# Performance work log

Measured on AMD Instinct MI355X. Metric: run time of the kernel, lower is better.

The kernel has to match this reference:

```python
import jax, jax.numpy as jnp
import numpy as np

K = 3  # kernel side; ori_col = K*K = 9


def _build_tpcms():
    # order-2: all pairs (i, j), i <= j, over the 9 patch positions
    pairs2 = []
    idx2 = {}
    c = 0
    for i in range(K * K):
        for j in range(i, K * K):
            pairs2.append((i, j))
            idx2[(i, j)] = c
            c += 1
    # order-3: (raw column index i, index of (j, k) in the order-2 tensor), i <= j <= k
    pairs3 = [(i, idx2[(j, k)])
              for i in range(K * K)
              for j in range(i, K * K)
              for k in range(j, K * K)]
    return np.asarray(pairs2, np.int32), np.asarray(pairs3, np.int32)


def setup_inputs() -> dict:
    key = jax.random.key(0)
    x = jax.random.normal(key, (4, 8, 128, 128), dtype=jnp.float32)
    p2, p3 = _build_tpcms()
    return {"x": x, "tpcm2": jnp.asarray(p2), "tpcm3": jnp.asarray(p3)}


def _unfold3x3(x):
    # torch.nn.Unfold(kernel=3, stride=1, pad=1) then view(B, C, 9, L):
    # per channel, the 9 kernel offsets are row-major (kh, kw).
    B, C, H, W = x.shape
    xp = jnp.pad(x, ((0, 0), (0, 0), (1, 1), (1, 1)))
    cols = [xp[:, :, i:i + H, j:j + W] for i in range(K) for j in range(K)]
    return jnp.stack(cols, axis=2).reshape(B, C, K * K, H * W)  # [B, C, 9, L]


def reference(x, tpcm2, tpcm3):
    Col = _unfold3x3(x)                                          # [B, C, 9, L]
    ht2 = Col[:, :, tpcm2[:, 0], :] * Col[:, :, tpcm2[:, 1], :]  # [B, C, 45, L]
    ht3 = Col[:, :, tpcm3[:, 0], :] * ht2[:, :, tpcm3[:, 1], :]  # [B, C, 165, L]
    return jnp.concatenate([ht2, ht3], axis=2)                   # [B, C, 210, L]
```

## Files before the change

### kernel.cpp

```cpp
#include <hip/hip_runtime.h>


#define HH 128
#define WW 128
#define LL (HH * WW)
#define NCH 210

__global__ __launch_bounds__(256) void hoi_kernel(const float* __restrict__ x,
                                                  float* __restrict__ out) {
    const int tid   = blockIdx.x * 256 + threadIdx.x;
    const int wq    = tid & 31;
    const int h     = (tid >> 5) & 127;
    const int plane = tid >> 12;
    const int w0    = wq << 2;

    const float* __restrict__ xp = x + (size_t)plane * LL;

    float r[3][6];
#pragma unroll
    for (int dh = 0; dh < 3; ++dh) {
        const int hh = h + dh - 1;
        const bool hv = (hh >= 0) & (hh < HH);
#pragma unroll
        for (int dw = 0; dw < 6; ++dw) {
            const int ww = w0 + dw - 1;
            const bool wv = (ww >= 0) & (ww < WW);
            r[dh][dw] = (hv & wv) ? xp[hh * WW + ww] : 0.0f;
        }
    }

    float4 v[9];
#pragma unroll
    for (int dh = 0; dh < 3; ++dh) {
#pragma unroll
        for (int dw = 0; dw < 3; ++dw) {
            v[dh * 3 + dw] = make_float4(r[dh][dw], r[dh][dw + 1],
                                         r[dh][dw + 2], r[dh][dw + 3]);
        }
    }

    float* __restrict__ obase = out + (size_t)plane * NCH * LL + h * WW + w0;
    int ch = 0;

#pragma unroll
    for (int i = 0; i < 9; ++i) {
#pragma unroll
        for (int j = i; j < 9; ++j) {
            float4 p;
            p.x = v[i].x * v[j].x;
            p.y = v[i].y * v[j].y;
            p.z = v[i].z * v[j].z;
            p.w = v[i].w * v[j].w;
            *reinterpret_cast<float4*>(obase + (size_t)ch * LL) = p;
            ++ch;
        }
    }

#pragma unroll
    for (int i = 0; i < 9; ++i) {
#pragma unroll
        for (int j = i; j < 9; ++j) {
#pragma unroll
            for (int k = j; k < 9; ++k) {
                float4 q;
                q.x = v[i].x * (v[j].x * v[k].x);
                q.y = v[i].y * (v[j].y * v[k].y);
                q.z = v[i].z * (v[j].z * v[k].z);
                q.w = v[i].w * (v[j].w * v[k].w);
                *reinterpret_cast<float4*>(obase + (size_t)ch * LL) = q;
                ++ch;
            }
        }
    }
}

extern "C" void kernel_launch(void* const* d_in, const int* in_sizes, int n_in,
                              void* d_out, int out_size, void* d_ws, size_t ws_size,
                              hipStream_t stream) {
    const float* x = (const float*)d_in[0];
    float* out = (float*)d_out;

    const int nplanes = in_sizes[0] / LL;
    const int total   = nplanes * HH * (WW / 4);
    const int block   = 256;
    const int grid    = (total + block - 1) / block;

    hoi_kernel<<<grid, block, 0, stream>>>(x, out);
}
```

Measured before the change: 434.0 us.

## Split channel work across a second grid dimension and reuse pair products for triples

Measured after the change: 432.7 us. Within noise of the previous version (-0.3%).

```diff
diff --git a/kernel.cpp b/kernel.cpp
--- a/kernel.cpp
+++ b/kernel.cpp
@@ -6,8 +6,44 @@
 #define LL (HH * WW)
 #define NCH 210
 
-__global__ __launch_bounds__(256) void hoi_kernel(const float* __restrict__ x,
-                                                  float* __restrict__ out) {
+__host__ __device__ constexpr int ch2_idx(int i, int j) {
+    return i * 9 - (i * (i - 1)) / 2 + (j - i);
+}
+__host__ __device__ constexpr int tri(int m) { return m * (m + 1) / 2; }
+__host__ __device__ constexpr int ch3_idx(int i, int j, int k) {
+    int s = 0;
+    for (int a = 0; a < i; ++a) s += tri(9 - a);
+    for (int b = i; b < j; ++b) s += (9 - b);
+    return 45 + s + (k - j);
+}
+
+template <int JLO, int JHI>
+__device__ __forceinline__ void emit(const float4 (&v)[9], float* __restrict__ obase) {
+#pragma unroll
+    for (int j = JLO; j < JHI; ++j) {
+#pragma unroll
+        for (int k = j; k < 9; ++k) {
+            float4 t;
+            t.x = v[j].x * v[k].x;
+            t.y = v[j].y * v[k].y;
+            t.z = v[j].z * v[k].z;
+            t.w = v[j].w * v[k].w;
+            *reinterpret_cast<float4*>(obase + ch2_idx(j, k) * LL) = t;
+#pragma unroll
+            for (int i = 0; i <= j; ++i) {
+                float4 q;
+                q.x = v[i].x * t.x;
+                q.y = v[i].y * t.y;
+                q.z = v[i].z * t.z;
+                q.w = v[i].w * t.w;
+                *reinterpret_cast<float4*>(obase + ch3_idx(i, j, k) * LL) = q;
+            }
+        }
+    }
+}
+
+__global__ __launch_bounds__(256, 4) void hoi_kernel(const float* __restrict__ x,
+                                                     float* __restrict__ out) {
     const int tid   = blockIdx.x * 256 + threadIdx.x;
     const int wq    = tid & 31;
     const int h     = (tid >> 5) & 127;
@@ -40,37 +76,11 @@
     }
 
     float* __restrict__ obase = out + (size_t)plane * NCH * LL + h * WW + w0;
-    int ch = 0;
 
-#pragma unroll
-    for (int i = 0; i < 9; ++i) {
-#pragma unroll
-        for (int j = i; j < 9; ++j) {
-            float4 p;
-            p.x = v[i].x * v[j].x;
-            p.y = v[i].y * v[j].y;
-            p.z = v[i].z * v[j].z;
-            p.w = v[i].w * v[j].w;
-            *reinterpret_cast<float4*>(obase + (size_t)ch * LL) = p;
-            ++ch;
-        }
-    }
-
-#pragma unroll
-    for (int i = 0; i < 9; ++i) {
-#pragma unroll
-        for (int j = i; j < 9; ++j) {
-#pragma unroll
-            for (int k = j; k < 9; ++k) {
-                float4 q;
-                q.x = v[i].x * (v[j].x * v[k].x);
-                q.y = v[i].y * (v[j].y * v[k].y);
-                q.z = v[i].z * (v[j].z * v[k].z);
-                q.w = v[i].w * (v[j].w * v[k].w);
-                *reinterpret_cast<float4*>(obase + (size_t)ch * LL) = q;
-                ++ch;
-            }
-        }
+    if (blockIdx.y == 0) {
+        emit<0, 4>(v, obase);
+    } else {
+        emit<4, 9>(v, obase);
     }
 }
 
@@ -83,7 +93,7 @@
     const int nplanes = in_sizes[0] / LL;
     const int total   = nplanes * HH * (WW / 4);
     const int block   = 256;
-    const int grid    = (total + block - 1) / block;
+    const int gx      = (total + block - 1) / block;
 
-    hoi_kernel<<<grid, block, 0, stream>>>(x, out);
+    hoi_kernel<<<dim3(gx, 2), block, 0, stream>>>(x, out);
 }
```
